# Performance work log

Measured on AMD Instinct MI355X. Metric: run time of the kernel, lower is better.

## Reference

```python
import jax, jax.numpy as jnp
import numpy as np
from jax import lax

IMG = 1280.0          # image side (80 * stride 16)
HF = WF = 80          # feature map
STRIDE = 16
A = 15                # anchors per location (5 sizes x 3 ratios)
KMIX = 5              # MDN mixture components
NIMG = 8
NGT = 32
PRE_NMS = 2000
POST_NMS = 1000
NMS_THRESH = 0.7
BATCH_PER_IMG = 256
POS_FRAC = 0.5
SCALE_CLAMP = float(np.log(1000.0 / 16.0))
LOG2PI = float(np.log(2.0 * np.pi))


def _make_anchors():
    sizes = np.array([32., 64., 128., 256., 512.])
    ratios = np.array([0.5, 1.0, 2.0])
    ws = (sizes[:, None] * np.sqrt(1.0 / ratios)[None, :]).reshape(-1)
    hs = (sizes[:, None] * np.sqrt(ratios)[None, :]).reshape(-1)
    base = np.stack([-ws / 2, -hs / 2, ws / 2, hs / 2], 1)  # [A,4]
    xs = (np.arange(WF) + 0.5) * STRIDE
    ys = (np.arange(HF) + 0.5) * STRIDE
    sx, sy = np.meshgrid(xs, ys)
    shifts = np.stack([sx.ravel(), sy.ravel(), sx.ravel(), sy.ravel()], 1)  # [HW,4]
    return jnp.asarray((shifts[:, None, :] + base[None]).reshape(-1, 4), jnp.float32)


def setup_inputs() -> dict:
    key = jax.random.key(0)
    k = jax.random.split(key, 6)
    R = HF * WF * A
    anchors = _make_anchors()                                                # [R,4]
    pi = jax.random.normal(k[0], (NIMG, KMIX, R), jnp.float32)
    mu = jax.random.normal(k[1], (NIMG, KMIX, R), jnp.float32)
    sigma = jax.random.uniform(k[2], (NIMG, KMIX, R), jnp.float32, 0.1, 1.0)
    deltas = jax.random.normal(k[3], (NIMG, R, 4), jnp.float32) * 0.1
    xy = jax.random.uniform(k[4], (NIMG, NGT, 2), jnp.float32, 0.0, 960.0)
    wh = jax.random.uniform(k[5], (NIMG, NGT, 2), jnp.float32, 20.0, 320.0)
    gt_boxes = jnp.concatenate([xy, xy + wh], -1)                            # [N,G,4]
    return {"anchors": anchors, "pi": pi, "mu": mu, "sigma": sigma,
            "deltas": deltas, "gt_boxes": gt_boxes}


def pairwise_iou(a, b):  # [M,4],[P,4] -> [M,P]
    area_a = (a[:, 2] - a[:, 0]) * (a[:, 3] - a[:, 1])
    area_b = (b[:, 2] - b[:, 0]) * (b[:, 3] - b[:, 1])
    lt = jnp.maximum(a[:, None, :2], b[None, :, :2])
    rb = jnp.minimum(a[:, None, 2:], b[None, :, 2:])
    wh = jnp.clip(rb - lt, 0.0)
    inter = wh[..., 0] * wh[..., 1]
    return inter / jnp.maximum(area_a[:, None] + area_b[None, :] - inter, 1e-9)


def apply_deltas(d, boxes):  # Box2BoxTransform.apply_deltas, weights=(1,1,1,1)
    w = boxes[:, 2] - boxes[:, 0]
    h = boxes[:, 3] - boxes[:, 1]
    cx = boxes[:, 0] + 0.5 * w
    cy = boxes[:, 1] + 0.5 * h
    dx, dy = d[:, 0], d[:, 1]
    dw = jnp.minimum(d[:, 2], SCALE_CLAMP)
    dh = jnp.minimum(d[:, 3], SCALE_CLAMP)
    pcx = dx * w + cx
    pcy = dy * h + cy
    pw = jnp.exp(dw) * w
    ph = jnp.exp(dh) * h
    return jnp.stack([pcx - 0.5 * pw, pcy - 0.5 * ph, pcx + 0.5 * pw, pcy + 0.5 * ph], 1)


def get_deltas(src, tgt):  # Box2BoxTransform.get_deltas
    sw = src[..., 2] - src[..., 0]
    sh = src[..., 3] - src[..., 1]
    scx = src[..., 0] + 0.5 * sw
    scy = src[..., 1] + 0.5 * sh
    tw = tgt[..., 2] - tgt[..., 0]
    th = tgt[..., 3] - tgt[..., 1]
    tcx = tgt[..., 0] + 0.5 * tw
    tcy = tgt[..., 1] + 0.5 * th
    return jnp.stack([(tcx - scx) / sw, (tcy - scy) / sh,
                      jnp.log(tw / sw), jnp.log(th / sh)], -1)


def _nms_image(boxes, scores, unc):  # [R,4],[R],[R,2] -> padded top proposals
    top_s, tidx = lax.top_k(scores, PRE_NMS)
    tb = jnp.clip(boxes[tidx], 0.0, IMG)   # clip to image
    tu = unc[tidx]
    iou = pairwise_iou(tb, tb)             # [PRE,PRE]
    ar = jnp.arange(PRE_NMS)

    def body(i, keep):
        sup = (iou[i] > NMS_THRESH) & (ar > i) & keep[i]
        return keep & ~sup

    keep = lax.fori_loop(0, PRE_NMS, body, jnp.ones((PRE_NMS,), bool))
    wv = tb[:, 2] - tb[:, 0]
    hv = tb[:, 3] - tb[:, 1]
    keep = keep & (wv > 0.0) & (hv > 0.0)  # min_box_size = 0
    ms = jnp.where(keep, top_s, -jnp.inf)
    out_s, oidx = lax.top_k(ms, POST_NMS)
    return tb[oidx], out_s, tu[oidx]


def _losses(anchors, pi, mu, sigma, deltas, gt_boxes):
    # label_and_sample_anchors (no_grad in torch)
    iou = lax.stop_gradient(jax.vmap(lambda g: pairwise_iou(g, anchors))(gt_boxes))  # [N,G,R]
    vals = iou.max(axis=1)                       # matched IoU quality  [N,R]
    idx = jnp.argmax(iou, axis=1)                # matched gt index     [N,R]
    labels = jnp.where(vals >= 0.7, 1, jnp.where(vals >= 0.3, -1, 0))
    best_gt = iou.max(axis=2)                    # [N,G]
    lq = jnp.any((iou >= best_gt[:, :, None] - 1e-7) & (best_gt[:, :, None] > 0), axis=1)
    labels = jnp.where(lq, 1, labels)            # allow_low_quality_matches
    # deterministic subsample to batch_size_per_image with positive_fraction
    pos = labels == 1
    neg = labels == 0
    n_pos = jnp.minimum(pos.sum(1), int(BATCH_PER_IMG * POS_FRAC))
    keep_pos = pos & (jnp.cumsum(pos, 1) <= n_pos[:, None])
    keep_neg = neg & (jnp.cumsum(neg, 1) <= (BATCH_PER_IMG - n_pos)[:, None])
    labels = jnp.where(keep_pos, 1, jnp.where(keep_neg, 0, -1))
    matched_gt = lax.stop_gradient(jax.vmap(lambda g, i: g[i])(gt_boxes, idx))  # [N,R,4]
    gt_deltas = get_deltas(lax.stop_gradient(anchors)[None], matched_gt)
    pos_mask = labels == 1
    # smooth_l1 with beta=0 -> L1, summed over positives
    loss_loc = jnp.sum(jnp.abs(deltas - gt_deltas) * pos_mask[..., None])
    valid = labels != -1
    t = jnp.clip(vals, 0.0, 1.0)
    lp = jax.nn.log_softmax(pi, axis=1)
    comp = lp - 0.5 * ((t[:, None, :] - mu) / sigma) ** 2 - jnp.log(sigma) - 0.5 * LOG2PI
    nll = -jax.nn.logsumexp(comp, axis=1)        # [N,R]
    loss_cls = jnp.sum(nll * valid)
    norm = BATCH_PER_IMG * pi.shape[0]
    return jnp.stack([loss_cls / norm, loss_loc / norm])


def reference(anchors, pi, mu, sigma, deltas, gt_boxes):
    # find_logit: pi-weighted mixture mean as objectness score
    pi_sm = jax.nn.softmax(pi, axis=1)           # [N,K,R]
    logits = jnp.sum(pi_sm * mu, axis=1)         # [N,R]
    # mdn_uncertainties: epistemic / aleatoric
    epis = jnp.sum(pi_sm * (mu - logits[:, None, :]) ** 2, axis=1)
    alea = jnp.sum(pi_sm * sigma ** 2, axis=1)
    unc = jnp.stack([epis, alea], -1)            # [N,R,2]
    # _decode_proposals
    boxes = jax.vmap(lambda d: apply_deltas(d, anchors))(deltas)  # [N,R,4]
    # find_top_rpn_proposals_uncertainty (pre-NMS topk, clip, NMS, post-NMS topk)
    prop_b, prop_s, prop_u = jax.vmap(_nms_image)(boxes, logits, unc)
    losses = _losses(anchors, pi, mu, sigma, deltas, gt_boxes)    # [loss_cls, loss_loc]
    return prop_b, prop_s, prop_u, losses
```

## Files before the change

### kernel.cpp

```cpp
#include <hip/hip_runtime.h>
#include <cstdint>
#include <cstddef>

typedef unsigned long long u64;
typedef unsigned int u32;
typedef unsigned short u16;
typedef unsigned char u8;

#define R_ANCH 96000
#define R4     24000
#define NIMG   8
#define KMIX   5
#define PRE    2000
#define POST   1000
#define NGT    32
#define NCHUNK 375
#define ACHUNK 94
#define NBLK   48
#define MROW   2048
#define SCAP   16
#define BIG_TH 64
#define CAP_BIN 6144
#define CAND_CAP 8192
#define GC_STRIDE 16

#define IMG_SZ        1280.0f
#define NMS_T         0.7f
#define SCALE_CLAMP_F 4.135166556742356f
#define HALF_L2PI     0.9189385332046727f

__device__ __forceinline__ u64 make_key(float s, int r) {
  u32 u = __float_as_uint(s);
  u = (u & 0x80000000u) ? ~u : (u | 0x80000000u);
  return ((u64)u << 32) | (u64)(0xFFFFFFFFu - (u32)r);
}

__device__ __forceinline__ float dec_score(u64 key) {
  u32 o = (u32)(key >> 32);
  u32 bits = (o & 0x80000000u) ? (o ^ 0x80000000u) : ~o;
  return __uint_as_float(bits);
}

__device__ __forceinline__ float iou_pair(float a0,float a1,float a2,float a3,
                                          float b0,float b1,float b2,float b3) {
#pragma clang fp contract(off)
  float areaA = (a2-a0)*(a3-a1);
  float areaB = (b2-b0)*(b3-b1);
  float lx=fmaxf(a0,b0), ly=fmaxf(a1,b1);
  float rx=fminf(a2,b2), ry=fminf(a3,b3);
  float iw=fmaxf(rx-lx,0.0f), ih=fmaxf(ry-ly,0.0f);
  float inter=iw*ih;
  return inter / fmaxf(areaA+areaB-inter, 1e-9f);
}

__device__ __forceinline__ void pick2048(const u32* __restrict__ hist, int k,
                                         int* s_i, u32* s_u,
                                         int& d_out, int& k_out, u32& cnt_out) {
  int tid = threadIdx.x;
  int lane = tid & 63, w = tid >> 6;
  u32 h[8]; u32 ssum = 0;
#pragma unroll
  for (int i=0;i<8;++i){ h[i] = hist[2047 - (tid*8 + i)]; ssum += h[i]; }
  u32 incl = ssum;
  for (int off=1; off<64; off<<=1){
    u32 t = (u32)__shfl_up((int)incl, off, 64);
    if (lane >= off) incl += t;
  }
  if (lane==63) s_i[w] = (int)incl;
  __syncthreads();
  u32 base = 0;
  for (int ww=0; ww<w; ++ww) base += (u32)s_i[ww];
  u32 run = base + incl - ssum;
#pragma unroll
  for (int i=0;i<8;++i){
    u32 nr = run + h[i];
    if (run < (u32)k && nr >= (u32)k){
      s_u[0] = (u32)(2047 - (tid*8+i));
      s_u[1] = (u32)k - run;
      s_u[2] = h[i];
    }
    run = nr;
  }
  __syncthreads();
  d_out = (int)s_u[0]; k_out = (int)s_u[1]; cnt_out = s_u[2];
  __syncthreads();
}

__device__ __forceinline__ void scan2048_desc(const u32* __restrict__ h,
                                              u32* __restrict__ off,
                                              u32* __restrict__ wsum, int tid) {
  int b_hi = 2047 - 2*tid, b_lo = b_hi - 1;
  u32 h_hi = h[b_hi], h_lo = h[b_lo];
  u32 sum = h_hi + h_lo;
  u32 incl = sum;
  int lane = tid & 63, wv = tid >> 6;
  for (int o=1; o<64; o<<=1){
    u32 t = (u32)__shfl_up((int)incl, o, 64);
    if (lane >= o) incl += t;
  }
  if (lane==63) wsum[wv] = incl;
  __syncthreads();
  u32 base = 0;
  for (int w=0; w<wv; ++w) base += wsum[w];
  u32 excl = base + incl - sum;
  off[b_hi] = excl;
  off[b_lo] = excl + h_hi;
}

__global__ void kZero(u32* z, int nwords) {
  for (int i = blockIdx.x*256 + threadIdx.x; i < nwords; i += gridDim.x*256)
    z[i] = 0u;
}

__global__ __launch_bounds__(256) void kA_mdn(
    const float* __restrict__ pi, const float* __restrict__ mu,
    const float* __restrict__ sigma, float* __restrict__ logits,
    float* __restrict__ epis, float* __restrict__ alea,
    u32* __restrict__ hist0,
    const float* __restrict__ anchors, const float* __restrict__ gt,
    int* __restrict__ best) {
  __shared__ u32 s_h[2048];
  __shared__ float s_gt[NGT*4];
  __shared__ float s_ga[NGT];
  __shared__ int s_best[NGT];
  int tid = threadIdx.x;
  int img = blockIdx.y;

  if (blockIdx.x >= ACHUNK) {
    int bx = blockIdx.x - ACHUNK;
    if (tid < NGT*4) s_gt[tid] = gt[img*NGT*4 + tid];
    if (tid < NGT){
      const float* g4 = gt + img*NGT*4 + tid*4;
      s_ga[tid] = (g4[2]-g4[0])*(g4[3]-g4[1]);
      s_best[tid] = 0;
    }
    __syncthreads();
    float4 an[8]; float aA[8];
#pragma unroll
    for (int q=0; q<8; ++q){
      int r = bx*256 + tid + q*(NBLK*256);
      an[q] = (r < R_ANCH) ? ((const float4*)anchors)[r]
                           : make_float4(0.f,0.f,0.f,0.f);
      aA[q] = (an[q].z-an[q].x)*(an[q].w-an[q].y);
    }
    float vmax[NGT];
#pragma unroll 2
    for (int g=0; g<NGT; ++g){
      float g0=s_gt[g*4], g1=s_gt[g*4+1], g2=s_gt[g*4+2], g3=s_gt[g*4+3];
      float ga=s_ga[g];
      float bi=0.0f, bu=1.0f;
#pragma unroll
      for (int q=0; q<8; ++q){
        float lx=fmaxf(g0,an[q].x), ly=fmaxf(g1,an[q].y);
        float rx=fminf(g2,an[q].z), ry=fminf(g3,an[q].w);
        float iw=fmaxf(rx-lx,0.0f), ih=fmaxf(ry-ly,0.0f);
        float inter=iw*ih;
        float uni=fmaxf(ga+aA[q]-inter,1e-9f);
        if (inter*bu > bi*uni){ bi=inter; bu=uni; }
      }
      vmax[g] = bi/bu;
    }
    int lane = tid & 63;
#pragma unroll
    for (int g=0; g<NGT; ++g){
      float v = vmax[g];
      v = fmaxf(v, __shfl_xor(v, 1, 64));
      v = fmaxf(v, __shfl_xor(v, 2, 64));
      v = fmaxf(v, __shfl_xor(v, 4, 64));
      v = fmaxf(v, __shfl_xor(v, 8, 64));
      v = fmaxf(v, __shfl_xor(v,16, 64));
      v = fmaxf(v, __shfl_xor(v,32, 64));
      if (lane==0 && v > 0.0f) atomicMax(&s_best[g], __float_as_int(v));
    }
    __syncthreads();
    if (tid < NGT) atomicMax(&best[img*NGT + tid], s_best[tid]);
    return;
  }

  int r4 = blockIdx.x*256 + tid;
  bool act = (r4 < R4);
  for (int b=tid; b<2048; b+=256) s_h[b]=0u;
  float4 lg4, ep4, al4;
  u64 keys[4];
  if (act){
    const float4* pi4 = (const float4*)pi;
    const float4* mu4 = (const float4*)mu;
    const float4* sg4 = (const float4*)sigma;
    size_t base = (size_t)img*KMIX*R4 + r4;
    float4 p4[KMIX], m4[KMIX], s4[KMIX];
#pragma unroll
    for (int k=0;k<KMIX;k++){
      p4[k]=pi4[base+(size_t)k*R4];
      m4[k]=mu4[base+(size_t)k*R4];
      s4[k]=sg4[base+(size_t)k*R4];
    }
    float lg_[4], ep_[4], al_[4];
#pragma unroll
    for (int j=0;j<4;++j){
      float p[KMIX], m[KMIX], s[KMIX];
#pragma unroll
      for (int k=0;k<KMIX;k++){
        p[k] = (&p4[k].x)[j];
        m[k] = (&m4[k].x)[j];
        s[k] = (&s4[k].x)[j];
      }
      float mx = p[0];
#pragma unroll
      for (int k=1;k<KMIX;k++) mx = fmaxf(mx,p[k]);
      float e[KMIX]; float sum = 0.0f;
#pragma unroll
      for (int k=0;k<KMIX;k++){ e[k]=expf(p[k]-mx); sum += e[k]; }
      float w[KMIX]; float lg = 0.0f;
#pragma unroll
      for (int k=0;k<KMIX;k++){ w[k]=e[k]/sum; lg += w[k]*m[k]; }
      float ep = 0.0f, al = 0.0f;
#pragma unroll
      for (int k=0;k<KMIX;k++){ float d=m[k]-lg; ep += w[k]*d*d; al += w[k]*s[k]*s[k]; }
      lg_[j]=lg; ep_[j]=ep; al_[j]=al;
      keys[j] = make_key(lg, r4*4 + j);
    }
    lg4 = make_float4(lg_[0],lg_[1],lg_[2],lg_[3]);
    ep4 = make_float4(ep_[0],ep_[1],ep_[2],ep_[3]);
    al4 = make_float4(al_[0],al_[1],al_[2],al_[3]);
    size_t o4 = (size_t)img*R4 + r4;
    ((float4*)logits)[o4] = lg4;
    ((float4*)epis)[o4]   = ep4;
    ((float4*)alea)[o4]   = al4;
  }
  __syncthreads();
  if (act){
#pragma unroll
    for (int j=0;j<4;++j)
      atomicAdd(&s_h[(u32)(keys[j]>>53)], 1u);
  }
  __syncthreads();
  for (int b=tid; b<2048; b+=256){ u32 v=s_h[b]; if(v) atomicAdd(&hist0[img*2048+b], v); }
}

__global__ __launch_bounds__(256) void kP1(const float* __restrict__ logits,
                                           const u32* __restrict__ hist0,
                                           u32* __restrict__ hist1) {
  __shared__ u32 s_h[2048];
  __shared__ int s_i[8]; __shared__ u32 s_u[3];
  int img = blockIdx.y, tid = threadIdx.x;
  int d0,k0; u32 c0;
  pick2048(hist0 + img*2048, PRE, s_i, s_u, d0,k0,c0);
  if (c0 <= CAP_BIN) return;
  for (int b=tid; b<2048; b+=256) s_h[b]=0u;
  __syncthreads();
  const float* sc = logits + (size_t)img*R_ANCH;
  for (int r = blockIdx.x*256 + tid; r < R_ANCH; r += NBLK*256){
    u64 key = make_key(sc[r], r);
    if ((int)(key>>53) == d0) atomicAdd(&s_h[(u32)(key>>42)&2047u], 1u);
  }
  __syncthreads();
  for (int b=tid; b<2048; b+=256){ u32 v=s_h[b]; if(v) atomicAdd(&hist1[img*2048+b], v); }
}

__global__ __launch_bounds__(256) void kP2(const float* __restrict__ logits,
                                           const u32* __restrict__ hist0,
                                           const u32* __restrict__ hist1,
                                           u32* __restrict__ hist2) {
  __shared__ u32 s_h[2048];
  __shared__ int s_i[8]; __shared__ u32 s_u[3];
  int img = blockIdx.y, tid = threadIdx.x;
  int d0,k0; u32 c0;
  pick2048(hist0 + img*2048, PRE, s_i, s_u, d0,k0,c0);
  if (c0 <= CAP_BIN) return;
  int d1,k1; u32 c1;
  pick2048(hist1 + img*2048, k0, s_i, s_u, d1,k1,c1);
  if (c1 <= CAP_BIN) return;
  u64 p1 = ((u64)d0<<11) | (u64)d1;
  for (int b=tid; b<2048; b+=256) s_h[b]=0u;
  __syncthreads();
  const float* sc = logits + (size_t)img*R_ANCH;
  for (int r = blockIdx.x*256 + tid; r < R_ANCH; r += NBLK*256){
    u64 key = make_key(sc[r], r);
    if ((key>>42) == p1) atomicAdd(&s_h[(u32)(key>>31)&2047u], 1u);
  }
  __syncthreads();
  for (int b=tid; b<2048; b+=256){ u32 v=s_h[b]; if(v) atomicAdd(&hist2[img*2048+b], v); }
}

__global__ __launch_bounds__(256) void kGather(const float* __restrict__ logits,
    const u32* __restrict__ hist0, const u32* __restrict__ hist1,
    const u32* __restrict__ hist2, u64* __restrict__ cand, u32* __restrict__ gcnt) {
  __shared__ int s_i[8]; __shared__ u32 s_u[3];
  __shared__ u64 s_cand[2048];
  __shared__ u32 s_cnt, s_base;
  int img = blockIdx.y, tid = threadIdx.x;
  if (tid==0) s_cnt = 0u;
  int d,kk; u32 c;
  pick2048(hist0 + img*2048, PRE, s_i, s_u, d,kk,c);
  u64 p = (u64)d; int L = 0;
  if (c > CAP_BIN){
    pick2048(hist1 + img*2048, kk, s_i, s_u, d,kk,c);
    p = (p<<11)|(u64)d; L = 1;
    if (c > CAP_BIN){
      pick2048(hist2 + img*2048, kk, s_i, s_u, d,kk,c);
      p = (p<<11)|(u64)d; L = 2;
    }
  }
  u64 T = p << (64 - 11*(L+1));
  const float* sc = logits + (size_t)img*R_ANCH;
  int lane = tid & 63;
  for (int r = blockIdx.x*256 + tid; r < R_ANCH; r += NBLK*256){
    u64 key = make_key(sc[r], r);
    bool take = (key >= T);
    u64 b = __ballot(take);
    if (b){
      u32 base = 0;
      if (lane==0) base = atomicAdd(&s_cnt, (u32)__popcll(b));
      base = (u32)__shfl((int)base, 0, 64);
      if (take){
        u32 pos = base + (u32)__popcll(b & ((1ull<<lane)-1ull));
        if (pos < 2048u) s_cand[pos] = key;
        else {
          u32 gp = atomicAdd(&gcnt[img*GC_STRIDE], 1u);
          if (gp < CAND_CAP) cand[(size_t)img*CAND_CAP + gp] = key;
        }
      }
    }
  }
  __syncthreads();
  u32 n = s_cnt < 2048u ? s_cnt : 2048u;
  if (tid==0) s_base = atomicAdd(&gcnt[img*GC_STRIDE], n);
  __syncthreads();
  u32 gb = s_base;
  for (u32 i=tid; i<n; i+=256)
    cand[(size_t)img*CAND_CAP + gb + i] = s_cand[i];
}

__global__ __launch_bounds__(1024) void kRank(
    const u64* __restrict__ cand, const u32* __restrict__ gcnt,
    const float* __restrict__ epis, const float* __restrict__ alea,
    const float* __restrict__ deltas, const float* __restrict__ anchors,
    float* __restrict__ tb, float* __restrict__ tu, float* __restrict__ ts) {
  __shared__ u64 s_key[CAND_CAP];
  __shared__ u16 s_idx0[CAND_CAP];
  __shared__ u16 s_idx1[CAND_CAP];
  __shared__ u32 s_h0[2048];
  __shared__ u32 s_off0[2048];
  __shared__ u32 s_h1[2048];
  __shared__ u32 s_off1[2048];
  __shared__ u32 s_wsum[16];
  __shared__ u32 s_nbig;
  __shared__ u16 s_big[128];
  int tid = threadIdx.x, img = blockIdx.x;
  u32 cnt = gcnt[img*GC_STRIDE];
  if (cnt > (u32)CAND_CAP) cnt = CAND_CAP;
  const u64* cp = cand + (size_t)img*CAND_CAP;
  for (int i=tid; i<CAND_CAP; i+=1024) s_key[i] = (i < (int)cnt) ? cp[i] : 0ull;
  for (int b=tid; b<2048; b+=1024){ s_h0[b] = 0u; }
  if (tid==0) s_nbig = 0u;
  __syncthreads();
  for (int i=tid; i<(int)cnt; i+=1024)
    atomicAdd(&s_h0[(u32)(s_key[i]>>53)], 1u);
  __syncthreads();
  scan2048_desc(s_h0, s_off0, s_wsum, tid);
  __syncthreads();
  for (int b=tid; b<2048; b+=1024){
    u32 sz = s_h0[b];
    if (sz > BIG_TH && s_off0[b] < PRE){
      u32 q = atomicAdd(&s_nbig, 1u);
      if (q < 128u) s_big[q] = (u16)b;
    }
  }
  __syncthreads();
  for (int i=tid; i<(int)cnt; i+=1024){
    u32 d = (u32)(s_key[i]>>53);
    u32 slot = atomicAdd(&s_off0[d], 1u);
    s_idx0[slot] = (u16)i;
  }
  __syncthreads();
  auto emit = [&](u64 my, u32 rank){
    if (rank < PRE){
      int p = (int)rank;
      u32 idx = 0xFFFFFFFFu - (u32)(my & 0xFFFFFFFFull);
      ts[img*PRE + p] = dec_score(my);
      float4 a = ((const float4*)anchors)[idx];
      float4 dd = ((const float4*)deltas)[(size_t)img*R_ANCH + idx];
      float w = a.z - a.x, h = a.w - a.y;
      float cx = a.x + 0.5f*w, cy = a.y + 0.5f*h;
      float dw = fminf(dd.z, SCALE_CLAMP_F), dh = fminf(dd.w, SCALE_CLAMP_F);
      float pcx = dd.x*w + cx, pcy = dd.y*h + cy;
      float pw = expf(dw)*w, ph = expf(dh)*h;
      float x0 = fminf(fmaxf(pcx - 0.5f*pw, 0.0f), IMG_SZ);
      float y0 = fminf(fmaxf(pcy - 0.5f*ph, 0.0f), IMG_SZ);
      float x1 = fminf(fmaxf(pcx + 0.5f*pw, 0.0f), IMG_SZ);
      float y1 = fminf(fmaxf(pcy + 0.5f*ph, 0.0f), IMG_SZ);
      ((float4*)tb)[(size_t)img*PRE + p] = make_float4(x0,y0,x1,y1);
      size_t o = (size_t)img*R_ANCH + idx;
      ((float2*)tu)[(size_t)img*PRE + p] = make_float2(epis[o], alea[o]);
    }
  };
  for (int i=tid; i<(int)cnt; i+=1024){
    u64 my = s_key[i];
    u32 d = (u32)(my>>53);
    u32 size = s_h0[d];
    if (size > BIG_TH) continue;
    u32 bs = s_off0[d] - size;
    if (bs >= PRE) continue;
    u32 rank = bs;
    for (u32 q=bs; q<bs+size; ++q)
      rank += (s_key[s_idx0[q]] > my) ? 1u : 0u;
    emit(my, rank);
  }
  __syncthreads();
  u32 nbig = s_nbig < 128u ? s_nbig : 128u;
  for (u32 bb=0; bb<nbig; ++bb){
    u32 B = s_big[bb];
    u32 size = s_h0[B];
    u32 base0 = s_off0[B] - size;
    for (int b=tid; b<2048; b+=1024) s_h1[b] = 0u;
    __syncthreads();
    for (u32 q=tid; q<size; q+=1024){
      u64 k = s_key[s_idx0[base0+q]];
      atomicAdd(&s_h1[(u32)(k>>42)&2047u], 1u);
    }
    __syncthreads();
    scan2048_desc(s_h1, s_off1, s_wsum, tid);
    __syncthreads();
    for (u32 q=tid; q<size; q+=1024){
      u16 ci = s_idx0[base0+q];
      u64 k = s_key[ci];
      u32 slot = atomicAdd(&s_off1[(u32)(k>>42)&2047u], 1u);
      s_idx1[slot] = ci;
    }
    __syncthreads();
    for (u32 q=tid; q<size; q+=1024){
      u16 ci = s_idx1[q];
      u64 my = s_key[ci];
      u32 d1 = (u32)(my>>42)&2047u;
      u32 ssz = s_h1[d1];
      u32 sbs = s_off1[d1] - ssz;
      u32 rank = base0 + sbs;
      for (u32 t2=sbs; t2<sbs+ssz; ++t2)
        rank += (s_key[s_idx1[t2]] > my) ? 1u : 0u;
      emit(my, rank);
    }
    __syncthreads();
  }
}

__global__ __launch_bounds__(1024) void kD_mask(const float* __restrict__ tb,
                                                u64* __restrict__ maskLT,
                                                u32* __restrict__ scnt,
                                                u16* __restrict__ slist) {
  __shared__ float4 s_tile[64];
  int tid = threadIdx.x;
  int a = blockIdx.x, img = blockIdx.y;
  const float4* tbi = (const float4*)tb + (size_t)img*PRE;
  if (tid < 64){
    int i = a*64 + tid;
    s_tile[tid] = (i < PRE) ? tbi[i] : make_float4(0.f,0.f,0.f,0.f);
  }
  __syncthreads();
  u64* outp = maskLT + ((size_t)img*32 + a)*MROW;
  u32* cnts = scnt + (size_t)img*2048;
  u16* lst  = slist + (size_t)img*2048*SCAP;
  int bmax = min(64, PRE - a*64);
  for (int j = a*64 + tid; j < MROW; j += 1024){
    u64 m = 0ull;
    if (j < PRE){
      float4 B = tbi[j];
      int blim = min(bmax, j - a*64);
      for (int b = 0; b < blim; ++b){
        float4 A = s_tile[b];
        float v = iou_pair(A.x,A.y,A.z,A.w, B.x,B.y,B.z,B.w);
        m |= (u64)(v > NMS_T) << b;
      }
    }
    outp[j] = m;
    u64 mm = m;
    while (mm){
      int b = __builtin_ctzll(mm); mm &= mm - 1ull;
      u32 slot = atomicAdd(&cnts[j], 1u);
      if (slot < SCAP) lst[(size_t)j*SCAP + slot] = (u16)(a*64 + b);
    }
  }
}

__global__ __launch_bounds__(1024) void kEF_nms(const u64* __restrict__ maskLT,
    const u32* __restrict__ scnt, const u16* __restrict__ slist,
    const float* __restrict__ tb, const float* __restrict__ tu,
    const float* __restrict__ ts, const float* __restrict__ acc,
    float* __restrict__ out) {
  __shared__ u64 s_list64[2048*SCAP/4];
  __shared__ u16 s_cnt[2048];
  __shared__ u8  kbuf[2][2048];
  __shared__ u64 s_kw[32];
  __shared__ int s_change, s_ovf;
  __shared__ int s_wk[16], s_wn[16];
  __shared__ int s_kc, s_runk, s_runn;
  int img = blockIdx.x, tid = threadIdx.x;
  int lane = tid & 63, wid = tid >> 6;
  const u64* gl = (const u64*)(slist + (size_t)img*2048*SCAP);
  for (int i=tid; i<2048*SCAP/4; i+=1024) s_list64[i] = gl[i];
  const u32* gc = scnt + (size_t)img*2048;
  for (int i=tid; i<2048; i+=1024) s_cnt[i] = (u16)gc[i];
  if (tid==0){ s_change = 0; s_ovf = 0; }
  __syncthreads();
  bool myovf = false;
#pragma unroll
  for (int q=0; q<2; ++q){
    int j = tid + q*1024;
    if (s_cnt[j] > SCAP) myovf = true;
    kbuf[0][j] = (j < PRE) ? 1 : 0;
  }
  if (myovf) s_ovf = 1;
  __syncthreads();
  const u64* MT = maskLT + (size_t)img*32*MROW;
  int cur = 0;
  for (int iter=0; iter<2048; ++iter){
    bool ovf = (s_ovf != 0);
    if (ovf && tid < 32){
      u64 w = 0ull;
      for (int b=0; b<64; ++b) w |= (u64)(kbuf[cur][tid*64+b] & 1) << b;
      s_kw[tid] = w;
    }
    __syncthreads();
    bool changed = false;
#pragma unroll
    for (int q=0; q<2; ++q){
      int j = tid + q*1024;
      u8 old = kbuf[cur][j];
      u8 nk = (j < PRE) ? 1 : 0;
      if (nk){
        int cnt = s_cnt[j];
        if (cnt <= SCAP){
          const u16* lp = (const u16*)&s_list64[j*(SCAP/4)];
          for (int i=0; i<cnt; ++i){
            if (kbuf[cur][lp[i]]){ nk = 0; break; }
          }
        } else {
          int amax = j >> 6;
          for (int a=0; a<=amax; ++a){
            if (MT[(size_t)a*MROW + j] & s_kw[a]){ nk = 0; break; }
          }
        }
      }
      kbuf[1-cur][j] = nk;
      changed |= (nk != old);
    }
    if (changed) s_change = 1;
    __syncthreads();
    int ch = s_change;
    __syncthreads();
    if (tid==0) s_change = 0;
    if (!ch) break;
    cur ^= 1;
  }
  __syncthreads();
  const float4* tbi = (const float4*)tb + (size_t)img*PRE;
  const float NEG_INF = __uint_as_float(0xff800000u);
  u8* kf = kbuf[1-cur];
#pragma unroll
  for (int cch=0; cch<2; ++cch){
    int pp = cch*1024 + tid;
    bool kp = false;
    if (pp < PRE && kbuf[cur][pp]){
      float4 b = tbi[pp];
      kp = (b.z > b.x) && (b.w > b.y);
    }
    kf[pp] = kp ? 1 : 0;
  }
  __syncthreads();
  {
    int cc = (int)kf[tid] + (int)kf[1024 + tid];
    for (int of=32; of>0; of>>=1) cc += __shfl_down(cc, of, 64);
    if (lane==0) s_wk[wid] = cc;
  }
  __syncthreads();
  if (tid==0){
    int t=0; for (int w=0; w<16; ++w) t += s_wk[w];
    s_kc = t; s_runk = 0; s_runn = 0;
  }
  __syncthreads();
  int kc = s_kc;
#pragma unroll
  for (int cch=0; cch<2; ++cch){
    int pp = cch*1024 + tid;
    bool kp = kf[pp] != 0;
    u64 bk = __ballot(kp), bn = __ballot(!kp);
    if (lane==0){ s_wk[wid]=__popcll(bk); s_wn[wid]=__popcll(bn); }
    __syncthreads();
    int pk = s_runk, pn = s_runn;
    for (int w=0; w<wid; ++w){ pk += s_wk[w]; pn += s_wn[w]; }
    u64 lm = (1ull<<lane) - 1ull;
    pk += __popcll(bk & lm);
    pn += __popcll(bn & lm);
    int slot = kp ? pk : (kc + pn);
    if (slot < POST && pp < PRE){
      ((float4*)out)[img*POST + slot] = tbi[pp];
      out[32000 + img*POST + slot] = kp ? ts[img*PRE + pp] : NEG_INF;
      ((float2*)(out + 40000))[img*POST + slot] = ((const float2*)tu)[(size_t)img*PRE + pp];
    }
    __syncthreads();
    if (tid==0){
      int tk=0, tn=0;
      for (int w=0; w<16; ++w){ tk += s_wk[w]; tn += s_wn[w]; }
      s_runk += tk; s_runn += tn;
    }
    __syncthreads();
  }
  if (img==0 && tid<2) out[56000+tid] = acc[tid] * (1.0f/2048.0f);
}

__global__ __launch_bounds__(256) void kL2_label(
    const float* __restrict__ anchors, const float* __restrict__ gt,
    const int* __restrict__ best,
    signed char* __restrict__ label, int* __restrict__ cpos, int* __restrict__ cneg) {
  __shared__ float s_gt[NGT*4];
  __shared__ float s_ga[NGT];
  __shared__ float s_bg[NGT];
  __shared__ int s_w[8];
  int tid = threadIdx.x, img = blockIdx.y;
  int r = blockIdx.x*256 + tid;
  if (tid < NGT*4) s_gt[tid] = gt[img*NGT*4 + tid];
  if (tid < NGT){
    const float* g4 = gt + img*NGT*4 + tid*4;
    s_ga[tid] = (g4[2]-g4[0])*(g4[3]-g4[1]);
    s_bg[tid] = __int_as_float(best[img*NGT + tid]);
  }
  __syncthreads();
  float4 a = ((const float4*)anchors)[r];
  float aA = (a.z-a.x)*(a.w-a.y);
  float bi=-1.0f, bu=1.0f; bool lq = false;
#pragma unroll 4
  for (int g=0; g<NGT; ++g){
    float g0=s_gt[g*4], g1=s_gt[g*4+1], g2=s_gt[g*4+2], g3=s_gt[g*4+3];
    float lx=fmaxf(g0,a.x), ly=fmaxf(g1,a.y);
    float rx=fminf(g2,a.z), ry=fminf(g3,a.w);
    float iw=fmaxf(rx-lx,0.0f), ih=fmaxf(ry-ly,0.0f);
    float inter=iw*ih;
    float uni = fmaxf(s_ga[g] + aA - inter, 1e-9f);
    if (inter*bu > bi*uni){ bi=inter; bu=uni; }
    float bg = s_bg[g];
    lq = lq || ((inter >= (bg - 1e-7f)*uni) && (bg > 0.0f));
  }
  float vbest = bi/bu;
  int lab = lq ? 1 : (vbest >= 0.7f ? 1 : (vbest >= 0.3f ? -1 : 0));
  label[(size_t)img*R_ANCH + r] = (signed char)lab;
  u64 bp = __ballot(lab==1), bn = __ballot(lab==0);
  int wid = tid>>6, lane = tid&63;
  if (lane==0){ s_w[wid*2]=__popcll(bp); s_w[wid*2+1]=__popcll(bn); }
  __syncthreads();
  if (tid==0){
    cpos[img*NCHUNK + blockIdx.x] = s_w[0]+s_w[2]+s_w[4]+s_w[6];
    cneg[img*NCHUNK + blockIdx.x] = s_w[1]+s_w[3]+s_w[5]+s_w[7];
  }
}

__global__ __launch_bounds__(256) void kL4_accum(
    const signed char* __restrict__ label,
    const float* __restrict__ pi, const float* __restrict__ mu,
    const float* __restrict__ sigma, const float* __restrict__ anchors,
    const float* __restrict__ gt, const float* __restrict__ deltas,
    const int* __restrict__ cpos, const int* __restrict__ cneg,
    float* __restrict__ acc) {
  __shared__ int s_wp[4], s_wn[4];
  __shared__ int s_r[12];
  __shared__ float s_red[8];
  __shared__ float s_gt[NGT*4];
  int tid = threadIdx.x, img = blockIdx.y, bx = blockIdx.x;
  int lane = tid & 63, wid = tid >> 6;
  if (tid < NGT*4) s_gt[tid] = gt[img*NGT*4 + tid];
  int vp=0, vn=0, tp=0;
  for (int k=tid; k<NCHUNK; k+=256){
    int cp = cpos[img*NCHUNK + k];
    int cn = cneg[img*NCHUNK + k];
    tp += cp;
    if (k < bx){ vp += cp; vn += cn; }
  }
  for (int of=32; of>0; of>>=1){
    vp += __shfl_down(vp, of, 64);
    vn += __shfl_down(vn, of, 64);
    tp += __shfl_down(tp, of, 64);
  }
  if (lane==0){ s_r[wid]=vp; s_r[4+wid]=vn; s_r[8+wid]=tp; }
  __syncthreads();
  int pre_p = s_r[0]+s_r[1]+s_r[2]+s_r[3];
  int pre_n = s_r[4]+s_r[5]+s_r[6]+s_r[7];
  int totp  = s_r[8]+s_r[9]+s_r[10]+s_r[11];
  int np = totp < 128 ? totp : 128;
  int nn = 256 - np;
  int r = bx*256 + tid;
  size_t o = (size_t)img*R_ANCH + r;
  int lab = label[o];
  bool pos = (lab==1), neg = (lab==0);
  u64 bp = __ballot(pos), bn = __ballot(neg);
  if (lane==0){ s_wp[wid]=__popcll(bp); s_wn[wid]=__popcll(bn); }
  __syncthreads();
  for (int w=0; w<wid; ++w){ pre_p += s_wp[w]; pre_n += s_wn[w]; }
  u64 lm = (1ull<<lane) - 1ull;
  pre_p += __popcll(bp & lm);
  pre_n += __popcll(bn & lm);
  bool kp = pos && (pre_p < np);
  bool kn = neg && (pre_n < nn);
  float c_cls = 0.0f, c_loc = 0.0f;
  if (kp || kn){
    float4 a = ((const float4*)anchors)[r];
    float aA = (a.z-a.x)*(a.w-a.y);
    float bi = -1.0f, bu = 1.0f; int idx = 0;
#pragma unroll 4
    for (int g=0; g<NGT; ++g){
      float g0=s_gt[g*4], g1=s_gt[g*4+1], g2=s_gt[g*4+2], g3=s_gt[g*4+3];
      float ga=(g2-g0)*(g3-g1);
      float lx=fmaxf(g0,a.x), ly=fmaxf(g1,a.y);
      float rx=fminf(g2,a.z), ry=fminf(g3,a.w);
      float iw=fmaxf(rx-lx,0.0f), ih=fmaxf(ry-ly,0.0f);
      float inter=iw*ih;
      float uni = fmaxf(ga + aA - inter, 1e-9f);
      if (inter*bu > bi*uni){ bi=inter; bu=uni; idx=g; }
    }
    float vbest = bi/bu;
    size_t base = (size_t)img*KMIX*R_ANCH + r;
    float p[KMIX], m[KMIX], s[KMIX];
#pragma unroll
    for (int k=0;k<KMIX;k++){
      p[k]=pi[base+(size_t)k*R_ANCH];
      m[k]=mu[base+(size_t)k*R_ANCH];
      s[k]=sigma[base+(size_t)k*R_ANCH];
    }
    float mx = p[0];
#pragma unroll
    for (int k=1;k<KMIX;k++) mx = fmaxf(mx,p[k]);
    float e[KMIX]; float sum = 0.0f;
#pragma unroll
    for (int k=0;k<KMIX;k++){ e[k]=expf(p[k]-mx); sum += e[k]; }
    float lsum = logf(sum);
    float t_ = fminf(fmaxf(vbest, 0.0f), 1.0f);
    float comp[KMIX];
#pragma unroll
    for (int k=0;k<KMIX;k++){
      float z = (t_ - m[k]) / s[k];
      comp[k] = (p[k]-mx-lsum) - 0.5f*z*z - logf(s[k]) - HALF_L2PI;
    }
    float cm = comp[0];
#pragma unroll
    for (int k=1;k<KMIX;k++) cm = fmaxf(cm, comp[k]);
    float se = 0.0f;
#pragma unroll
    for (int k=0;k<KMIX;k++) se += expf(comp[k]-cm);
    c_cls = -(cm + logf(se));
    if (kp){
      const float* gb = &s_gt[idx*4];
      float sw = a.z-a.x, sh = a.w-a.y;
      float scx = a.x+0.5f*sw, scy = a.y+0.5f*sh;
      float tw = gb[2]-gb[0], th = gb[3]-gb[1];
      float tcx = gb[0]+0.5f*tw, tcy = gb[1]+0.5f*th;
      float4 d = ((const float4*)deltas)[(size_t)img*R_ANCH + r];
      c_loc = fabsf(d.x-(tcx-scx)/sw) + fabsf(d.y-(tcy-scy)/sh)
            + fabsf(d.z-logf(tw/sw)) + fabsf(d.w-logf(th/sh));
    }
  }
  for (int of=32; of>0; of>>=1){
    c_cls += __shfl_down(c_cls, of, 64);
    c_loc += __shfl_down(c_loc, of, 64);
  }
  if (lane==0){ s_red[wid]=c_cls; s_red[4+wid]=c_loc; }
  __syncthreads();
  if (tid==0){
    float a = s_red[0]+s_red[1]+s_red[2]+s_red[3];
    float b = s_red[4]+s_red[5]+s_red[6]+s_red[7];
    if (a != 0.0f) atomicAdd(&acc[0], a);
    if (b != 0.0f) atomicAdd(&acc[1], b);
  }
}

extern "C" void kernel_launch(void* const* d_in, const int* in_sizes, int n_in,
                              void* d_out, int out_size, void* d_ws, size_t ws_size,
                              hipStream_t stream) {
  const float* anchors = (const float*)d_in[0];
  const float* pi      = (const float*)d_in[1];
  const float* mu      = (const float*)d_in[2];
  const float* sigma   = (const float*)d_in[3];
  const float* deltas  = (const float*)d_in[4];
  const float* gt      = (const float*)d_in[5];
  float* out = (float*)d_out;

  char* ws = (char*)d_ws;
  size_t off = 0;
  auto alloc = [&](size_t bytes) -> void* {
    void* p = (void*)(ws + off);
    off += (bytes + 255) & ~(size_t)255;
    return p;
  };
  float* logits = (float*)alloc((size_t)NIMG*R_ANCH*4);
  float* epis   = (float*)alloc((size_t)NIMG*R_ANCH*4);
  float* alea   = (float*)alloc((size_t)NIMG*R_ANCH*4);
  float* tb     = (float*)alloc((size_t)NIMG*PRE*4*4);
  float* tu     = (float*)alloc((size_t)NIMG*PRE*2*4);
  float* ts     = (float*)alloc((size_t)NIMG*PRE*4);
  u64*   maskLT = (u64*)  alloc((size_t)NIMG*32*MROW*8);
  u16*   slist  = (u16*)  alloc((size_t)NIMG*2048*SCAP*2);
  u64*   cand   = (u64*)  alloc((size_t)NIMG*CAND_CAP*8);
  int*   cpos   = (int*)  alloc((size_t)NIMG*NCHUNK*4);
  int*   cneg   = (int*)  alloc((size_t)NIMG*NCHUNK*4);
  size_t zstart = off;
  u32*   hist0  = (u32*)  alloc((size_t)NIMG*2048*4);
  u32*   hist1  = (u32*)  alloc((size_t)NIMG*2048*4);
  u32*   hist2  = (u32*)  alloc((size_t)NIMG*2048*4);
  u32*   gcnt   = (u32*)  alloc((size_t)NIMG*GC_STRIDE*4);
  int*   best   = (int*)  alloc((size_t)NIMG*NGT*4);
  u32*   scnt   = (u32*)  alloc((size_t)NIMG*2048*4);
  float* acc    = (float*)alloc(8);
  int zwords = (int)((off - zstart) / 4);
  signed char* label = (signed char*)logits;

  kZero<<<dim3(64), dim3(256), 0, stream>>>((u32*)(ws + zstart), zwords);
  kA_mdn<<<dim3(ACHUNK+NBLK, NIMG), dim3(256), 0, stream>>>(pi, mu, sigma, logits, epis, alea,
                                                            hist0, anchors, gt, best);
  kP1<<<dim3(NBLK, NIMG), dim3(256), 0, stream>>>(logits, hist0, hist1);
  kP2<<<dim3(NBLK, NIMG), dim3(256), 0, stream>>>(logits, hist0, hist1, hist2);
  kGather<<<dim3(NBLK, NIMG), dim3(256), 0, stream>>>(logits, hist0, hist1, hist2, cand, gcnt);
  kRank<<<dim3(NIMG), dim3(1024), 0, stream>>>(cand, gcnt, epis, alea, deltas, anchors, tb, tu, ts);
  kD_mask<<<dim3(32, NIMG), dim3(1024), 0, stream>>>(tb, maskLT, scnt, slist);
  kL2_label<<<dim3(NCHUNK, NIMG), dim3(256), 0, stream>>>(anchors, gt, best, label, cpos, cneg);
  kL4_accum<<<dim3(NCHUNK, NIMG), dim3(256), 0, stream>>>(label, pi, mu, sigma, anchors, gt, deltas,
                                                          cpos, cneg, acc);
  kEF_nms<<<dim3(NIMG), dim3(1024), 0, stream>>>(maskLT, scnt, slist, tb, tu, ts, acc, out);
}
```

Measured before the change: 263.4 us.

## Fold loss labeling and accumulation into top-k select kernels as extra blocks

The anchor labeling kernel is merged into the first radix-histogram pass and the loss accumulation kernel into the gather pass, as extra blocks beyond the original grid. This removes two launches and lets the loss work run alongside the narrow top-k select kernels, filling otherwise idle CUs. Labels move to their own workspace buffer because they can no longer alias logits, which the concurrent select blocks still read. Risks are larger shared-memory footprints from the union of both block types and a heavier kP1 that always launches the extra blocks.

Result: no change. 259.9 us (-1.3%).

```diff
diff --git a/kernel.cpp b/kernel.cpp
--- a/kernel.cpp
+++ b/kernel.cpp
@@ -237,12 +237,58 @@
   for (int b=tid; b<2048; b+=256){ u32 v=s_h[b]; if(v) atomicAdd(&hist0[img*2048+b], v); }
 }
 
-__global__ __launch_bounds__(256) void kP1(const float* __restrict__ logits,
-                                           const u32* __restrict__ hist0,
-                                           u32* __restrict__ hist1) {
+__global__ __launch_bounds__(256) void kP1L2(const float* __restrict__ logits,
+    const u32* __restrict__ hist0, u32* __restrict__ hist1,
+    const float* __restrict__ anchors, const float* __restrict__ gt,
+    const int* __restrict__ best,
+    signed char* __restrict__ label, int* __restrict__ cpos, int* __restrict__ cneg) {
+  int img = blockIdx.y, tid = threadIdx.x;
+
+  if (blockIdx.x >= NBLK) {
+    __shared__ float s_gt[NGT*4];
+    __shared__ float s_ga[NGT];
+    __shared__ float s_bg[NGT];
+    __shared__ int s_w[8];
+    int bx = blockIdx.x - NBLK;
+    int r = bx*256 + tid;
+    if (tid < NGT*4) s_gt[tid] = gt[img*NGT*4 + tid];
+    if (tid < NGT){
+      const float* g4 = gt + img*NGT*4 + tid*4;
+      s_ga[tid] = (g4[2]-g4[0])*(g4[3]-g4[1]);
+      s_bg[tid] = __int_as_float(best[img*NGT + tid]);
+    }
+    __syncthreads();
+    float4 a = ((const float4*)anchors)[r];
+    float aA = (a.z-a.x)*(a.w-a.y);
+    float bi=-1.0f, bu=1.0f; bool lq = false;
+#pragma unroll 4
+    for (int g=0; g<NGT; ++g){
+      float g0=s_gt[g*4], g1=s_gt[g*4+1], g2=s_gt[g*4+2], g3=s_gt[g*4+3];
+      float lx=fmaxf(g0,a.x), ly=fmaxf(g1,a.y);
+      float rx=fminf(g2,a.z), ry=fminf(g3,a.w);
+      float iw=fmaxf(rx-lx,0.0f), ih=fmaxf(ry-ly,0.0f);
+      float inter=iw*ih;
+      float uni = fmaxf(s_ga[g] + aA - inter, 1e-9f);
+      if (inter*bu > bi*uni){ bi=inter; bu=uni; }
+      float bg = s_bg[g];
+      lq = lq || ((inter >= (bg - 1e-7f)*uni) && (bg > 0.0f));
+    }
+    float vbest = bi/bu;
+    int lab = lq ? 1 : (vbest >= 0.7f ? 1 : (vbest >= 0.3f ? -1 : 0));
+    label[(size_t)img*R_ANCH + r] = (signed char)lab;
+    u64 bp = __ballot(lab==1), bn = __ballot(lab==0);
+    int wid = tid>>6, lane = tid&63;
+    if (lane==0){ s_w[wid*2]=__popcll(bp); s_w[wid*2+1]=__popcll(bn); }
+    __syncthreads();
+    if (tid==0){
+      cpos[img*NCHUNK + bx] = s_w[0]+s_w[2]+s_w[4]+s_w[6];
+      cneg[img*NCHUNK + bx] = s_w[1]+s_w[3]+s_w[5]+s_w[7];
+    }
+    return;
+  }
+
   __shared__ u32 s_h[2048];
   __shared__ int s_i[8]; __shared__ u32 s_u[3];
-  int img = blockIdx.y, tid = threadIdx.x;
   int d0,k0; u32 c0;
   pick2048(hist0 + img*2048, PRE, s_i, s_u, d0,k0,c0);
   if (c0 <= CAP_BIN) return;
@@ -282,13 +328,132 @@
   for (int b=tid; b<2048; b+=256){ u32 v=s_h[b]; if(v) atomicAdd(&hist2[img*2048+b], v); }
 }
 
-__global__ __launch_bounds__(256) void kGather(const float* __restrict__ logits,
+__global__ __launch_bounds__(256) void kGatherL4(const float* __restrict__ logits,
     const u32* __restrict__ hist0, const u32* __restrict__ hist1,
-    const u32* __restrict__ hist2, u64* __restrict__ cand, u32* __restrict__ gcnt) {
+    const u32* __restrict__ hist2, u64* __restrict__ cand, u32* __restrict__ gcnt,
+    const signed char* __restrict__ label,
+    const float* __restrict__ pi, const float* __restrict__ mu,
+    const float* __restrict__ sigma, const float* __restrict__ anchors,
+    const float* __restrict__ gt, const float* __restrict__ deltas,
+    const int* __restrict__ cpos, const int* __restrict__ cneg,
+    float* __restrict__ acc) {
+  int img = blockIdx.y, tid = threadIdx.x;
+
+  if (blockIdx.x >= NBLK) {
+    __shared__ int s_wp[4], s_wn[4];
+    __shared__ int s_r[12];
+    __shared__ float s_red[8];
+    __shared__ float s_gt[NGT*4];
+    int bx = blockIdx.x - NBLK;
+    int lane = tid & 63, wid = tid >> 6;
+    if (tid < NGT*4) s_gt[tid] = gt[img*NGT*4 + tid];
+    int vp=0, vn=0, tp=0;
+    for (int k=tid; k<NCHUNK; k+=256){
+      int cp = cpos[img*NCHUNK + k];
+      int cn = cneg[img*NCHUNK + k];
+      tp += cp;
+      if (k < bx){ vp += cp; vn += cn; }
+    }
+    for (int of=32; of>0; of>>=1){
+      vp += __shfl_down(vp, of, 64);
+      vn += __shfl_down(vn, of, 64);
+      tp += __shfl_down(tp, of, 64);
+    }
+    if (lane==0){ s_r[wid]=vp; s_r[4+wid]=vn; s_r[8+wid]=tp; }
+    __syncthreads();
+    int pre_p = s_r[0]+s_r[1]+s_r[2]+s_r[3];
+    int pre_n = s_r[4]+s_r[5]+s_r[6]+s_r[7];
+    int totp  = s_r[8]+s_r[9]+s_r[10]+s_r[11];
+    int np = totp < 128 ? totp : 128;
+    int nn = 256 - np;
+    int r = bx*256 + tid;
+    size_t o = (size_t)img*R_ANCH + r;
+    int lab = label[o];
+    bool pos = (lab==1), neg = (lab==0);
+    u64 bp = __ballot(pos), bn = __ballot(neg);
+    if (lane==0){ s_wp[wid]=__popcll(bp); s_wn[wid]=__popcll(bn); }
+    __syncthreads();
+    for (int w=0; w<wid; ++w){ pre_p += s_wp[w]; pre_n += s_wn[w]; }
+    u64 lm = (1ull<<lane) - 1ull;
+    pre_p += __popcll(bp & lm);
+    pre_n += __popcll(bn & lm);
+    bool kp = pos && (pre_p < np);
+    bool kn = neg && (pre_n < nn);
+    float c_cls = 0.0f, c_loc = 0.0f;
+    if (kp || kn){
+      float4 a = ((const float4*)anchors)[r];
+      float aA = (a.z-a.x)*(a.w-a.y);
+      float bi = -1.0f, bu = 1.0f; int idx = 0;
+#pragma unroll 4
+      for (int g=0; g<NGT; ++g){
+        float g0=s_gt[g*4], g1=s_gt[g*4+1], g2=s_gt[g*4+2], g3=s_gt[g*4+3];
+        float ga=(g2-g0)*(g3-g1);
+        float lx=fmaxf(g0,a.x), ly=fmaxf(g1,a.y);
+        float rx=fminf(g2,a.z), ry=fminf(g3,a.w);
+        float iw=fmaxf(rx-lx,0.0f), ih=fmaxf(ry-ly,0.0f);
+        float inter=iw*ih;
+        float uni = fmaxf(ga + aA - inter, 1e-9f);
+        if (inter*bu > bi*uni){ bi=inter; bu=uni; idx=g; }
+      }
+      float vbest = bi/bu;
+      size_t base = (size_t)img*KMIX*R_ANCH + r;
+      float p[KMIX], m[KMIX], s[KMIX];
+#pragma unroll
+      for (int k=0;k<KMIX;k++){
+        p[k]=pi[base+(size_t)k*R_ANCH];
+        m[k]=mu[base+(size_t)k*R_ANCH];
+        s[k]=sigma[base+(size_t)k*R_ANCH];
+      }
+      float mx = p[0];
+#pragma unroll
+      for (int k=1;k<KMIX;k++) mx = fmaxf(mx,p[k]);
+      float e[KMIX]; float sum = 0.0f;
+#pragma unroll
+      for (int k=0;k<KMIX;k++){ e[k]=expf(p[k]-mx); sum += e[k]; }
+      float lsum = logf(sum);
+      float t_ = fminf(fmaxf(vbest, 0.0f), 1.0f);
+      float comp[KMIX];
+#pragma unroll
+      for (int k=0;k<KMIX;k++){
+        float z = (t_ - m[k]) / s[k];
+        comp[k] = (p[k]-mx-lsum) - 0.5f*z*z - logf(s[k]) - HALF_L2PI;
+      }
+      float cm = comp[0];
+#pragma unroll
+      for (int k=1;k<KMIX;k++) cm = fmaxf(cm, comp[k]);
+      float se = 0.0f;
+#pragma unroll
+      for (int k=0;k<KMIX;k++) se += expf(comp[k]-cm);
+      c_cls = -(cm + logf(se));
+      if (kp){
+        const float* gb = &s_gt[idx*4];
+        float sw = a.z-a.x, sh = a.w-a.y;
+        float scx = a.x+0.5f*sw, scy = a.y+0.5f*sh;
+        float tw = gb[2]-gb[0], th = gb[3]-gb[1];
+        float tcx = gb[0]+0.5f*tw, tcy = gb[1]+0.5f*th;
+        float4 d = ((const float4*)deltas)[(size_t)img*R_ANCH + r];
+        c_loc = fabsf(d.x-(tcx-scx)/sw) + fabsf(d.y-(tcy-scy)/sh)
+              + fabsf(d.z-logf(tw/sw)) + fabsf(d.w-logf(th/sh));
+      }
+    }
+    for (int of=32; of>0; of>>=1){
+      c_cls += __shfl_down(c_cls, of, 64);
+      c_loc += __shfl_down(c_loc, of, 64);
+    }
+    if (lane==0){ s_red[wid]=c_cls; s_red[4+wid]=c_loc; }
+    __syncthreads();
+    if (tid==0){
+      float a = s_red[0]+s_red[1]+s_red[2]+s_red[3];
+      float b = s_red[4]+s_red[5]+s_red[6]+s_red[7];
+      if (a != 0.0f) atomicAdd(&acc[0], a);
+      if (b != 0.0f) atomicAdd(&acc[1], b);
+    }
+    return;
+  }
+
   __shared__ int s_i[8]; __shared__ u32 s_u[3];
   __shared__ u64 s_cand[2048];
   __shared__ u32 s_cnt, s_base;
-  int img = blockIdx.y, tid = threadIdx.x;
   if (tid==0) s_cnt = 0u;
   int d,kk; u32 c;
   pick2048(hist0 + img*2048, PRE, s_i, s_u, d,kk,c);
@@ -607,168 +772,6 @@
   if (img==0 && tid<2) out[56000+tid] = acc[tid] * (1.0f/2048.0f);
 }
 
-__global__ __launch_bounds__(256) void kL2_label(
-    const float* __restrict__ anchors, const float* __restrict__ gt,
-    const int* __restrict__ best,
-    signed char* __restrict__ label, int* __restrict__ cpos, int* __restrict__ cneg) {
-  __shared__ float s_gt[NGT*4];
-  __shared__ float s_ga[NGT];
-  __shared__ float s_bg[NGT];
-  __shared__ int s_w[8];
-  int tid = threadIdx.x, img = blockIdx.y;
-  int r = blockIdx.x*256 + tid;
-  if (tid < NGT*4) s_gt[tid] = gt[img*NGT*4 + tid];
-  if (tid < NGT){
-    const float* g4 = gt + img*NGT*4 + tid*4;
-    s_ga[tid] = (g4[2]-g4[0])*(g4[3]-g4[1]);
-    s_bg[tid] = __int_as_float(best[img*NGT + tid]);
-  }
-  __syncthreads();
-  float4 a = ((const float4*)anchors)[r];
-  float aA = (a.z-a.x)*(a.w-a.y);
-  float bi=-1.0f, bu=1.0f; bool lq = false;
-#pragma unroll 4
-  for (int g=0; g<NGT; ++g){
-    float g0=s_gt[g*4], g1=s_gt[g*4+1], g2=s_gt[g*4+2], g3=s_gt[g*4+3];
-    float lx=fmaxf(g0,a.x), ly=fmaxf(g1,a.y);
-    float rx=fminf(g2,a.z), ry=fminf(g3,a.w);
-    float iw=fmaxf(rx-lx,0.0f), ih=fmaxf(ry-ly,0.0f);
-    float inter=iw*ih;
-    float uni = fmaxf(s_ga[g] + aA - inter, 1e-9f);
-    if (inter*bu > bi*uni){ bi=inter; bu=uni; }
-    float bg = s_bg[g];
-    lq = lq || ((inter >= (bg - 1e-7f)*uni) && (bg > 0.0f));
-  }
-  float vbest = bi/bu;
-  int lab = lq ? 1 : (vbest >= 0.7f ? 1 : (vbest >= 0.3f ? -1 : 0));
-  label[(size_t)img*R_ANCH + r] = (signed char)lab;
-  u64 bp = __ballot(lab==1), bn = __ballot(lab==0);
-  int wid = tid>>6, lane = tid&63;
-  if (lane==0){ s_w[wid*2]=__popcll(bp); s_w[wid*2+1]=__popcll(bn); }
-  __syncthreads();
-  if (tid==0){
-    cpos[img*NCHUNK + blockIdx.x] = s_w[0]+s_w[2]+s_w[4]+s_w[6];
-    cneg[img*NCHUNK + blockIdx.x] = s_w[1]+s_w[3]+s_w[5]+s_w[7];
-  }
-}
-
-__global__ __launch_bounds__(256) void kL4_accum(
-    const signed char* __restrict__ label,
-    const float* __restrict__ pi, const float* __restrict__ mu,
-    const float* __restrict__ sigma, const float* __restrict__ anchors,
-    const float* __restrict__ gt, const float* __restrict__ deltas,
-    const int* __restrict__ cpos, const int* __restrict__ cneg,
-    float* __restrict__ acc) {
-  __shared__ int s_wp[4], s_wn[4];
-  __shared__ int s_r[12];
-  __shared__ float s_red[8];
-  __shared__ float s_gt[NGT*4];
-  int tid = threadIdx.x, img = blockIdx.y, bx = blockIdx.x;
-  int lane = tid & 63, wid = tid >> 6;
-  if (tid < NGT*4) s_gt[tid] = gt[img*NGT*4 + tid];
-  int vp=0, vn=0, tp=0;
-  for (int k=tid; k<NCHUNK; k+=256){
-    int cp = cpos[img*NCHUNK + k];
-    int cn = cneg[img*NCHUNK + k];
-    tp += cp;
-    if (k < bx){ vp += cp; vn += cn; }
-  }
-  for (int of=32; of>0; of>>=1){
-    vp += __shfl_down(vp, of, 64);
-    vn += __shfl_down(vn, of, 64);
-    tp += __shfl_down(tp, of, 64);
-  }
-  if (lane==0){ s_r[wid]=vp; s_r[4+wid]=vn; s_r[8+wid]=tp; }
-  __syncthreads();
-  int pre_p = s_r[0]+s_r[1]+s_r[2]+s_r[3];
-  int pre_n = s_r[4]+s_r[5]+s_r[6]+s_r[7];
-  int totp  = s_r[8]+s_r[9]+s_r[10]+s_r[11];
-  int np = totp < 128 ? totp : 128;
-  int nn = 256 - np;
-  int r = bx*256 + tid;
-  size_t o = (size_t)img*R_ANCH + r;
-  int lab = label[o];
-  bool pos = (lab==1), neg = (lab==0);
-  u64 bp = __ballot(pos), bn = __ballot(neg);
-  if (lane==0){ s_wp[wid]=__popcll(bp); s_wn[wid]=__popcll(bn); }
-  __syncthreads();
-  for (int w=0; w<wid; ++w){ pre_p += s_wp[w]; pre_n += s_wn[w]; }
-  u64 lm = (1ull<<lane) - 1ull;
-  pre_p += __popcll(bp & lm);
-  pre_n += __popcll(bn & lm);
-  bool kp = pos && (pre_p < np);
-  bool kn = neg && (pre_n < nn);
-  float c_cls = 0.0f, c_loc = 0.0f;
-  if (kp || kn){
-    float4 a = ((const float4*)anchors)[r];
-    float aA = (a.z-a.x)*(a.w-a.y);
-    float bi = -1.0f, bu = 1.0f; int idx = 0;
-#pragma unroll 4
-    for (int g=0; g<NGT; ++g){
-      float g0=s_gt[g*4], g1=s_gt[g*4+1], g2=s_gt[g*4+2], g3=s_gt[g*4+3];
-      float ga=(g2-g0)*(g3-g1);
-      float lx=fmaxf(g0,a.x), ly=fmaxf(g1,a.y);
-      float rx=fminf(g2,a.z), ry=fminf(g3,a.w);
-      float iw=fmaxf(rx-lx,0.0f), ih=fmaxf(ry-ly,0.0f);
-      float inter=iw*ih;
-      float uni = fmaxf(ga + aA - inter, 1e-9f);
-      if (inter*bu > bi*uni){ bi=inter; bu=uni; idx=g; }
-    }
-    float vbest = bi/bu;
-    size_t base = (size_t)img*KMIX*R_ANCH + r;
-    float p[KMIX], m[KMIX], s[KMIX];
-#pragma unroll
-    for (int k=0;k<KMIX;k++){
-      p[k]=pi[base+(size_t)k*R_ANCH];
-      m[k]=mu[base+(size_t)k*R_ANCH];
-      s[k]=sigma[base+(size_t)k*R_ANCH];
-    }
-    float mx = p[0];
-#pragma unroll
-    for (int k=1;k<KMIX;k++) mx = fmaxf(mx,p[k]);
-    float e[KMIX]; float sum = 0.0f;
-#pragma unroll
-    for (int k=0;k<KMIX;k++){ e[k]=expf(p[k]-mx); sum += e[k]; }
-    float lsum = logf(sum);
-    float t_ = fminf(fmaxf(vbest, 0.0f), 1.0f);
-    float comp[KMIX];
-#pragma unroll
-    for (int k=0;k<KMIX;k++){
-      float z = (t_ - m[k]) / s[k];
-      comp[k] = (p[k]-mx-lsum) - 0.5f*z*z - logf(s[k]) - HALF_L2PI;
-    }
-    float cm = comp[0];
-#pragma unroll
-    for (int k=1;k<KMIX;k++) cm = fmaxf(cm, comp[k]);
-    float se = 0.0f;
-#pragma unroll
-    for (int k=0;k<KMIX;k++) se += expf(comp[k]-cm);
-    c_cls = -(cm + logf(se));
-    if (kp){
-      const float* gb = &s_gt[idx*4];
-      float sw = a.z-a.x, sh = a.w-a.y;
-      float scx = a.x+0.5f*sw, scy = a.y+0.5f*sh;
-      float tw = gb[2]-gb[0], th = gb[3]-gb[1];
-      float tcx = gb[0]+0.5f*tw, tcy = gb[1]+0.5f*th;
-      float4 d = ((const float4*)deltas)[(size_t)img*R_ANCH + r];
-      c_loc = fabsf(d.x-(tcx-scx)/sw) + fabsf(d.y-(tcy-scy)/sh)
-            + fabsf(d.z-logf(tw/sw)) + fabsf(d.w-logf(th/sh));
-    }
-  }
-  for (int of=32; of>0; of>>=1){
-    c_cls += __shfl_down(c_cls, of, 64);
-    c_loc += __shfl_down(c_loc, of, 64);
-  }
-  if (lane==0){ s_red[wid]=c_cls; s_red[4+wid]=c_loc; }
-  __syncthreads();
-  if (tid==0){
-    float a = s_red[0]+s_red[1]+s_red[2]+s_red[3];
-    float b = s_red[4]+s_red[5]+s_red[6]+s_red[7];
-    if (a != 0.0f) atomicAdd(&acc[0], a);
-    if (b != 0.0f) atomicAdd(&acc[1], b);
-  }
-}
-
 extern "C" void kernel_launch(void* const* d_in, const int* in_sizes, int n_in,
                               void* d_out, int out_size, void* d_ws, size_t ws_size,
                               hipStream_t stream) {
@@ -790,6 +793,7 @@
   float* logits = (float*)alloc((size_t)NIMG*R_ANCH*4);
   float* epis   = (float*)alloc((size_t)NIMG*R_ANCH*4);
   float* alea   = (float*)alloc((size_t)NIMG*R_ANCH*4);
+  signed char* label = (signed char*)alloc((size_t)NIMG*R_ANCH);
   float* tb     = (float*)alloc((size_t)NIMG*PRE*4*4);
   float* tu     = (float*)alloc((size_t)NIMG*PRE*2*4);
   float* ts     = (float*)alloc((size_t)NIMG*PRE*4);
@@ -807,18 +811,17 @@
   u32*   scnt   = (u32*)  alloc((size_t)NIMG*2048*4);
   float* acc    = (float*)alloc(8);
   int zwords = (int)((off - zstart) / 4);
-  signed char* label = (signed char*)logits;
 
   kZero<<<dim3(64), dim3(256), 0, stream>>>((u32*)(ws + zstart), zwords);
   kA_mdn<<<dim3(ACHUNK+NBLK, NIMG), dim3(256), 0, stream>>>(pi, mu, sigma, logits, epis, alea,
                                                             hist0, anchors, gt, best);
-  kP1<<<dim3(NBLK, NIMG), dim3(256), 0, stream>>>(logits, hist0, hist1);
+  kP1L2<<<dim3(NBLK+NCHUNK, NIMG), dim3(256), 0, stream>>>(logits, hist0, hist1,
+                                                           anchors, gt, best, label, cpos, cneg);
   kP2<<<dim3(NBLK, NIMG), dim3(256), 0, stream>>>(logits, hist0, hist1, hist2);
-  kGather<<<dim3(NBLK, NIMG), dim3(256), 0, stream>>>(logits, hist0, hist1, hist2, cand, gcnt);
+  kGatherL4<<<dim3(NBLK+NCHUNK, NIMG), dim3(256), 0, stream>>>(logits, hist0, hist1, hist2,
+                                                               cand, gcnt, label, pi, mu, sigma,
+                                                               anchors, gt, deltas, cpos, cneg, acc);
   kRank<<<dim3(NIMG), dim3(1024), 0, stream>>>(cand, gcnt, epis, alea, deltas, anchors, tb, tu, ts);
   kD_mask<<<dim3(32, NIMG), dim3(1024), 0, stream>>>(tb, maskLT, scnt, slist);
-  kL2_label<<<dim3(NCHUNK, NIMG), dim3(256), 0, stream>>>(anchors, gt, best, label, cpos, cneg);
-  kL4_accum<<<dim3(NCHUNK, NIMG), dim3(256), 0, stream>>>(label, pi, mu, sigma, anchors, gt, deltas,
-                                                          cpos, cneg, acc);
   kEF_nms<<<dim3(NIMG), dim3(1024), 0, stream>>>(maskLT, scnt, slist, tb, tu, ts, acc, out);
 }
```
